# Performance work log

Hardware: AMD Instinct MI355X
Metric: run time of the kernel (lower is better)

Reference implementation:

```python
import jax, jax.numpy as jnp
import numpy as np

N = 65536          # query points (rays * samples per chunk)
C = 2048           # num_codes in code cloud
K = 16             # knn neighbors
CD = 64            # code_dim
IN_XYZ = 63        # positional-encoded xyz channels
IN_DIR = 27        # positional-encoded dir channels
W = 128            # decoder width (D=4, skips=[2])
DIST_SCALE = 2.0


def setup_inputs() -> dict:
    key = jax.random.key(0)
    ks = jax.random.split(key, 16)

    def glorot(k, shape):
        return jax.random.normal(k, shape, jnp.float32) / np.float32(np.sqrt(shape[0]))

    in_x = CD + IN_XYZ  # decoder in_channels_xyz = 127
    inp = {
        "indices": jnp.zeros((1,), jnp.int32),
        "query_points": jax.random.uniform(ks[0], (N, 3), jnp.float32),
        "xyzdir_embedded": jax.random.normal(ks[1], (N, IN_XYZ + IN_DIR), jnp.float32),
        "codes_position": jax.random.uniform(ks[2], (1, C, 3), jnp.float32),
        "codes": jax.random.normal(ks[3], (1, C, CD), jnp.float32) * 0.01,
        # decoder params
        "W0": glorot(ks[4], (in_x, W)), "b0": jnp.zeros((W,), jnp.float32),
        "W1": glorot(ks[5], (W, W)), "b1": jnp.zeros((W,), jnp.float32),
        "W2": glorot(ks[6], (W + in_x, W)), "b2": jnp.zeros((W,), jnp.float32),  # skip layer i=2
        "W3": glorot(ks[7], (W, W)), "b3": jnp.zeros((W,), jnp.float32),
        "Wf": glorot(ks[8], (W, W)), "bf": jnp.zeros((W,), jnp.float32),          # xyz_encoding_final
        "Wd": glorot(ks[9], (W + IN_DIR, W // 2)), "bd": jnp.zeros((W // 2,), jnp.float32),
        "Ws": glorot(ks[10], (W, 1)), "bs": jnp.zeros((1,), jnp.float32),
        "Wr": glorot(ks[11], (W // 2, 3)), "br": jnp.zeros((3,), jnp.float32),
    }
    return inp


def _knn_idx(q, c, k):
    # brute-force L2 knn (faiss replacement); indices only, no grad (torch no_grad)
    q = jax.lax.stop_gradient(q)
    c = jax.lax.stop_gradient(c)
    d2 = (jnp.sum(q * q, -1, keepdims=True)
          - 2.0 * q @ c.T
          + jnp.sum(c * c, -1))  # (N, C)
    _, idx = jax.lax.top_k(-d2, k)  # (N, K) nearest
    return idx


def reference(indices, query_points, xyzdir_embedded, codes_position, codes,
              W0, b0, W1, b1, W2, b2, W3, b3, Wf, bf, Wd, bd, Ws, bs, Wr, br):
    # --- CodeCloud.query ---
    cp = codes_position[indices][0]      # (C, 3)
    cc = codes[indices][0]               # (C, CD)
    idx = _knn_idx(query_points, cp, K)  # (N, K)
    neigh_pos = cp[idx]                  # (N, K, 3)
    sq = jnp.sum((query_points[:, None, :] - neigh_pos) ** 2, -1) + 1e-16  # (N, K)
    w = 1.0 / jnp.sqrt(sq) ** DIST_SCALE
    w = w / jnp.sum(w, -1, keepdims=True)
    neigh_codes = cc[idx]                # (N, K, CD)
    query_codes = jnp.einsum("nk,nkd->nd", w, neigh_codes)  # (N, CD)

    # --- IM_Decoder (D=4, W=128, skips=[2]) ---
    x = jnp.concatenate([query_codes, xyzdir_embedded], -1)  # (N, 127+27)
    in_x = CD + IN_XYZ
    input_xyz, input_dir = x[:, :in_x], x[:, in_x:]
    h = jax.nn.relu(input_xyz @ W0 + b0)
    h = jax.nn.relu(h @ W1 + b1)
    h = jax.nn.relu(jnp.concatenate([input_xyz, h], -1) @ W2 + b2)  # skip at i=2
    h = jax.nn.relu(h @ W3 + b3)
    sigma = h @ Ws + bs                       # (N, 1)
    final = h @ Wf + bf                       # (N, W)
    d = jax.nn.relu(jnp.concatenate([final, input_dir], -1) @ Wd + bd)
    rgb = d @ Wr + br                         # (N, 3)
    return jnp.concatenate([rgb, sigma], -1)  # (N, 4)
```

## Files before the change

kernel.cpp:

```cpp
#include <hip/hip_runtime.h>

#define N_Q   65536
#define N_C   2048
#define KNN_K 16
#define CDIM  64
#define SLCAP 64
#define KINF  0x7FFFFFFF

typedef _Float16 half_t;
typedef float v4f __attribute__((ext_vector_type(4)));
typedef half_t v8h __attribute__((ext_vector_type(8)));

#define ASTRIDE 136
#define DSTRIDE 40

__global__ void wtrans_kernel(const float* W0, const float* W1, const float* W2,
                              const float* W3, const float* Wf, const float* Wd,
                              const int* indices, const float* cpos,
                              half_t* wt, float4* cpos4){
  int idx = blockIdx.x * 256 + threadIdx.x;
  if (idx >= 110592) return;
  if (idx >= 108544){
    int i = idx - 108544;
    const float* cp = cpos + (size_t)indices[0] * N_C * 3;
    float x = cp[i*3 + 0], y = cp[i*3 + 1], z = cp[i*3 + 2];
    cpos4[i] = make_float4(x, y, z, fmaf(x, x, fmaf(y, y, fmaf(z, z, 4.0f))));
    return;
  }
  int base, nt, mode;
  const float* src = W1;
  if (idx < 16384){ base = 0; nt = 8; mode = 1; }
  else if (idx < 32768){ base = 16384; nt = 8; mode = 0; src = W1; }
  else if (idx < 65536){ base = 32768; nt = 8; mode = 2; }
  else if (idx < 81920){ base = 65536; nt = 8; mode = 0; src = W3; }
  else if (idx < 98304){ base = 81920; nt = 8; mode = 0; src = Wf; }
  else { base = 98304; nt = 4; mode = 3; }
  int i = idx - base;
  int tile = i >> 9, e = i & 511;
  int lane = e >> 3, j = e & 7;
  int k0idx = tile / nt, tcol = tile - k0idx*nt;
  int n = tcol*16 + (lane & 15);
  int k = k0idx*32 + ((lane >> 4) << 3) + j;
  float val;
  if (mode == 0)      val = src[k*128 + n];
  else if (mode == 1) val = (k < 127) ? W0[k*128 + n] : 0.f;
  else if (mode == 2) val = (k == 127) ? 0.f
                           : ((k < 127) ? W2[k*128 + n] : W2[(k-1)*128 + n]);
  else                val = (k < 155) ? Wd[k*64 + n] : 0.f;
  wt[idx] = (half_t)val;
}

__global__ void prep_kernel(const float* xyzdir, half_t* Ain, half_t* Din){
  int idx = blockIdx.x * 256 + threadIdx.x;
  if (idx < N_Q*72){
    int q = idx / 72, c = idx - q*72 + 64;
    float v = (c < 127) ? xyzdir[(size_t)q*90 + (c - 64)] : 0.f;
    Ain[(size_t)q*ASTRIDE + c] = (half_t)v;
  } else {
    int i2 = idx - N_Q*72;
    if (i2 >= N_Q*40) return;
    int q = i2 / 40, c = i2 - q*40;
    float v = (c < 27) ? xyzdir[(size_t)q*90 + 63 + c] : 0.f;
    Din[(size_t)q*DSTRIDE + c] = (half_t)v;
  }
}

__global__ __launch_bounds__(512, 8) void knn_kernel(const int* indices,
    const float* qpts, const float4* cpos4, const float* codes, half_t* Ain){
  __shared__ float4 lp[N_C];
  __shared__ int    sl[8*SLCAP];
  int tid = threadIdx.x;
  int lane = tid & 63, wave = tid >> 6;
  const float* cc = codes + (size_t)indices[0] * N_C * CDIM;

  for (int c = tid; c < N_C; c += 512) lp[c] = cpos4[c];
  __syncthreads();

  int q = blockIdx.x * 8 + wave;
  float qx = qpts[q*3 + 0];
  float qy = qpts[q*3 + 1];
  float qz = qpts[q*3 + 2];
  float nqx = -2.0f*qx, nqy = -2.0f*qy, nqz = -2.0f*qz;

  int p[32];
#pragma unroll
  for (int j = 0; j < 32; j++){
    int c = j*64 + lane;
    float4 P = lp[c];
    float s = fmaf(P.x, nqx, fmaf(P.y, nqy, fmaf(P.z, nqz, P.w)));
    p[j] = (__float_as_int(s) & 0xFFFFF800) | c;
  }

  int lm = p[0];
#pragma unroll
  for (int j = 1; j < 32; j++) lm = min(lm, p[j]);

  int v = lm;
#pragma unroll
  for (int k = 2; k <= 64; k <<= 1){
#pragma unroll
    for (int j = k >> 1; j > 0; j >>= 1){
      int o = __shfl_xor(v, j, 64);
      bool dirDesc = (lane & k) != 0;
      bool lower   = (lane & j) == 0;
      int mn = min(v, o), mx = max(v, o);
      v = (lower != dirDesc) ? mn : mx;
    }
  }
  int tau = __shfl(v, 15, 64);

  int cnt = 0;
#pragma unroll
  for (int j = 0; j < 32; j++) cnt += (p[j] <= tau) ? 1 : 0;
  int incl = cnt;
#pragma unroll
  for (int d = 1; d < 64; d <<= 1){
    int t = __shfl_up(incl, d, 64);
    incl += (lane >= d) ? t : 0;
  }
  int n = __shfl(incl, 63, 64);
  int base = incl - cnt;

  int keep = 0;
  if (n >= KNN_K && n <= SLCAP){
    int* slw = &sl[wave * SLCAP];
    int off = base;
#pragma unroll
    for (int j = 0; j < 32; j++){
      if (p[j] <= tau){ slw[off] = p[j]; off++; }
    }
    __builtin_amdgcn_wave_barrier();

    int x = (lane < n) ? slw[lane] : KINF;
#pragma unroll
    for (int k = 2; k <= 64; k <<= 1){
#pragma unroll
      for (int j = k >> 1; j > 0; j >>= 1){
        int o = __shfl_xor(x, j, 64);
        bool dirDesc = (lane & k) != 0;
        bool lower   = (lane & j) == 0;
        int mn = min(x, o), mx = max(x, o);
        x = (lower != dirDesc) ? mn : mx;
      }
    }
    keep = x;
  } else {
#pragma unroll 1
    for (int rr = 0; rr < KNN_K; rr++){
      int lmf = p[0];
#pragma unroll
      for (int j = 1; j < 32; j++) lmf = min(lmf, p[j]);
      int gm = lmf;
#pragma unroll
      for (int off2 = 1; off2 < 64; off2 <<= 1)
        gm = min(gm, __shfl_xor(gm, off2, 64));
      if (lane == rr) keep = gm;
#pragma unroll
      for (int j = 0; j < 32; j++) p[j] = (p[j] == gm) ? KINF : p[j];
    }
  }

  int ci = keep & 0x7FF;
  float4 P = lp[ci];
  float dx = qx - P.x, dy = qy - P.y, dz = qz - P.z;
  float d2 = fmaf(dz, dz, fmaf(dy, dy, dx*dx));
  float w = 1.0f / (d2 + 1e-16f);
  float wm = (lane < KNN_K) ? w : 0.0f;
#pragma unroll
  for (int off2 = 1; off2 < 64; off2 <<= 1) wm += __shfl_xor(wm, off2, 64);
  float wn = w / wm;

  float acc = 0.f;
#pragma unroll
  for (int i = 0; i < KNN_K; i++){
    int   cb = __shfl(ci, i, 64);
    float wb = __shfl(wn, i, 64);
    acc = fmaf(wb, cc[cb*CDIM + lane], acc);
  }
  Ain[(size_t)q*ASTRIDE + lane] = (half_t)acc;
}

template<int NT>
__device__ inline void mfma_sw(const half_t* act, int astride, int rowbase,
                               const half_t* wlayer, int nt, int ktbase,
                               int tcolbase, int kchunk, v4f* acc, int lane){
  int m = lane & 15, quad = lane >> 4;
#pragma unroll
  for (int k0 = 0; k0 < kchunk; k0 += 32){
    v8h a = *(const v8h*)&act[(rowbase + m)*astride + k0 + quad*8];
    int krow = ktbase + (k0 >> 5);
#pragma unroll
    for (int t = 0; t < NT; t++){
      const half_t* bp = wlayer + ((size_t)((krow*nt + tcolbase + t) << 9) + (lane << 3));
      v8h b = *(const v8h*)bp;
      acc[t] = __builtin_amdgcn_mfma_f32_16x16x32_f16(a, b, acc[t], 0, 0, 0);
    }
  }
}

template<int NT>
__device__ inline void epilogue(v4f* acc, half_t* outb, int rowbase, int colbase,
                                const float* bias, bool relu, int lane){
  int n = lane & 15, quad = lane >> 4;
#pragma unroll
  for (int t = 0; t < NT; t++){
    int col = colbase + t*16 + n;
    float bv = bias[col];
#pragma unroll
    for (int r = 0; r < 4; r++){
      float v = acc[t][r] + bv;
      if (relu) v = fmaxf(v, 0.f);
      outb[(rowbase + quad*4 + r)*ASTRIDE + col] = (half_t)v;
    }
  }
}

__global__ __launch_bounds__(256) void mlp_mfma(
    const half_t* Ain, const half_t* Din, const half_t* wt,
    const float* b0, const float* b1, const float* b2, const float* b3,
    const float* bfb, const float* bdb,
    const float* Wsb, const float* bsb, const float* Wrb, const float* brb,
    float* out){
  __shared__ __align__(16) half_t Abuf[32*ASTRIDE];
  __shared__ __align__(16) half_t Pbuf[32*ASTRIDE];
  __shared__ __align__(16) half_t Qbuf[32*ASTRIDE];
  __shared__ __align__(16) half_t Dbuf[32*DSTRIDE];

  int tid = threadIdx.x, lane = tid & 63, wave = tid >> 6;
  int qbase = blockIdx.x * 32;

  for (int i = tid; i < 32*17; i += 256){
    int r = i / 17, c8 = i - r*17;
    *(uint4*)&Abuf[r*ASTRIDE + (c8 << 3)] =
        *(const uint4*)&Ain[(size_t)(qbase + r)*ASTRIDE + (c8 << 3)];
  }
  for (int i = tid; i < 32*5; i += 256){
    int r = i / 5, c8 = i - r*5;
    *(uint4*)&Dbuf[r*DSTRIDE + (c8 << 3)] =
        *(const uint4*)&Din[(size_t)(qbase + r)*DSTRIDE + (c8 << 3)];
  }
  __syncthreads();

  int rowbase = (wave >> 1) * 16;
  int colhalf = wave & 1;
  int colbase = colhalf * 64;
  int tcolbase = colhalf * 4;
  v4f acc[4];

  const half_t* wt0 = wt;
  const half_t* wt1 = wt + 16384;
  const half_t* wt2 = wt + 32768;
  const half_t* wt3 = wt + 65536;
  const half_t* wtf = wt + 81920;
  const half_t* wtd = wt + 98304;

#define ZACC4() { for (int t_ = 0; t_ < 4; t_++) for (int e_ = 0; e_ < 4; e_++) acc[t_][e_] = 0.f; }

  ZACC4();
  mfma_sw<4>(Abuf, ASTRIDE, rowbase, wt0, 8, 0, tcolbase, 128, acc, lane);
  epilogue<4>(acc, Pbuf, rowbase, colbase, b0, true, lane);
  __syncthreads();

  ZACC4();
  mfma_sw<4>(Pbuf, ASTRIDE, rowbase, wt1, 8, 0, tcolbase, 128, acc, lane);
  epilogue<4>(acc, Qbuf, rowbase, colbase, b1, true, lane);
  __syncthreads();

  ZACC4();
  mfma_sw<4>(Abuf, ASTRIDE, rowbase, wt2, 8, 0, tcolbase, 128, acc, lane);
  mfma_sw<4>(Qbuf, ASTRIDE, rowbase, wt2, 8, 4, tcolbase, 128, acc, lane);
  epilogue<4>(acc, Pbuf, rowbase, colbase, b2, true, lane);
  __syncthreads();

  ZACC4();
  mfma_sw<4>(Pbuf, ASTRIDE, rowbase, wt3, 8, 0, tcolbase, 128, acc, lane);
  epilogue<4>(acc, Abuf, rowbase, colbase, b3, true, lane);
  __syncthreads();

  ZACC4();
  mfma_sw<4>(Abuf, ASTRIDE, rowbase, wtf, 8, 0, tcolbase, 128, acc, lane);
  epilogue<4>(acc, Pbuf, rowbase, colbase, bfb, false, lane);
  __syncthreads();

  int tcolbase_d = colhalf * 2;
  int colbase_d  = colhalf * 32;
  ZACC4();
  mfma_sw<2>(Pbuf, ASTRIDE, rowbase, wtd, 4, 0, tcolbase_d, 128, acc, lane);
  mfma_sw<2>(Dbuf, DSTRIDE, rowbase, wtd, 4, 4, tcolbase_d,  32, acc, lane);
  epilogue<2>(acc, Qbuf, rowbase, colbase_d, bdb, true, lane);
  __syncthreads();

  {
    int q = tid >> 3, part = tid & 7;
    float s = 0.f;
#pragma unroll
    for (int k = 0; k < 16; k++){
      int kk = part*16 + k;
      s = fmaf((float)Abuf[q*ASTRIDE + kk], Wsb[kk], s);
    }
    s += __shfl_xor(s, 1, 64); s += __shfl_xor(s, 2, 64); s += __shfl_xor(s, 4, 64);

    float r3[3];
#pragma unroll
    for (int c2 = 0; c2 < 3; c2++){
      float rv = 0.f;
#pragma unroll
      for (int k = 0; k < 8; k++){
        int kk = part*8 + k;
        rv = fmaf((float)Qbuf[q*ASTRIDE + kk], Wrb[kk*3 + c2], rv);
      }
      rv += __shfl_xor(rv, 1, 64); rv += __shfl_xor(rv, 2, 64); rv += __shfl_xor(rv, 4, 64);
      r3[c2] = rv;
    }
    if (part == 0){
      size_t ob = ((size_t)(qbase + q)) * 4;
      out[ob + 0] = r3[0] + brb[0];
      out[ob + 1] = r3[1] + brb[1];
      out[ob + 2] = r3[2] + brb[2];
      out[ob + 3] = s + bsb[0];
    }
  }
}

extern "C" void kernel_launch(void* const* d_in, const int* in_sizes, int n_in,
                              void* d_out, int out_size, void* d_ws, size_t ws_size,
                              hipStream_t stream){
  (void)in_sizes; (void)n_in; (void)out_size; (void)ws_size;

  const int*   indices = (const int*)d_in[0];
  const float* qpts    = (const float*)d_in[1];
  const float* xyzdir  = (const float*)d_in[2];
  const float* cpos    = (const float*)d_in[3];
  const float* codes   = (const float*)d_in[4];
  const float* W0 = (const float*)d_in[5];
  const float* b0 = (const float*)d_in[6];
  const float* W1 = (const float*)d_in[7];
  const float* b1 = (const float*)d_in[8];
  const float* W2 = (const float*)d_in[9];
  const float* b2 = (const float*)d_in[10];
  const float* W3 = (const float*)d_in[11];
  const float* b3 = (const float*)d_in[12];
  const float* Wf = (const float*)d_in[13];
  const float* bf = (const float*)d_in[14];
  const float* Wd = (const float*)d_in[15];
  const float* bd = (const float*)d_in[16];
  const float* Ws = (const float*)d_in[17];
  const float* bs = (const float*)d_in[18];
  const float* Wr = (const float*)d_in[19];
  const float* br = (const float*)d_in[20];

  half_t* Ain   = (half_t*)d_ws;
  half_t* Din   = (half_t*)((char*)d_ws + 17825792);
  half_t* wt    = (half_t*)((char*)d_ws + 17825792 + 5242880);
  float4* cpos4 = (float4*)((char*)d_ws + 17825792 + 5242880 + 217088);

  wtrans_kernel<<<(110592 + 255)/256, 256, 0, stream>>>(W0, W1, W2, W3, Wf, Wd,
                                                        indices, cpos, wt, cpos4);
  prep_kernel<<<(N_Q*112 + 255)/256, 256, 0, stream>>>(xyzdir, Ain, Din);
  knn_kernel<<<N_Q/8, 512, 0, stream>>>(indices, qpts, cpos4, codes, Ain);
  mlp_mfma<<<N_Q/32, 256, 0, stream>>>(Ain, Din, wt,
                                       b0, b1, b2, b3, bf, bd, Ws, bs, Wr, br,
                                       (float*)d_out);
}
```

Baseline: 243.1 us.

## Fuse input prep into knn kernel and cheapen threshold selection with ballot compaction

```diff
diff --git a/kernel.cpp b/kernel.cpp
--- a/kernel.cpp
+++ b/kernel.cpp
@@ -4,7 +4,7 @@
 #define N_C   2048
 #define KNN_K 16
 #define CDIM  64
-#define SLCAP 64
+#define SLCAP 128
 #define KINF  0x7FFFFFFF
 
 typedef _Float16 half_t;
@@ -50,27 +50,14 @@
   wt[idx] = (half_t)val;
 }
 
-__global__ void prep_kernel(const float* xyzdir, half_t* Ain, half_t* Din){
-  int idx = blockIdx.x * 256 + threadIdx.x;
-  if (idx < N_Q*72){
-    int q = idx / 72, c = idx - q*72 + 64;
-    float v = (c < 127) ? xyzdir[(size_t)q*90 + (c - 64)] : 0.f;
-    Ain[(size_t)q*ASTRIDE + c] = (half_t)v;
-  } else {
-    int i2 = idx - N_Q*72;
-    if (i2 >= N_Q*40) return;
-    int q = i2 / 40, c = i2 - q*40;
-    float v = (c < 27) ? xyzdir[(size_t)q*90 + 63 + c] : 0.f;
-    Din[(size_t)q*DSTRIDE + c] = (half_t)v;
-  }
-}
-
 __global__ __launch_bounds__(512, 8) void knn_kernel(const int* indices,
-    const float* qpts, const float4* cpos4, const float* codes, half_t* Ain){
+    const float* qpts, const float4* cpos4, const float* codes,
+    const float* xyzdir, half_t* Ain, half_t* Din){
   __shared__ float4 lp[N_C];
   __shared__ int    sl[8*SLCAP];
   int tid = threadIdx.x;
   int lane = tid & 63, wave = tid >> 6;
+  int l = lane & 15;
   const float* cc = codes + (size_t)indices[0] * N_C * CDIM;
 
   for (int c = tid; c < N_C; c += 512) lp[c] = cpos4[c];
@@ -97,54 +84,65 @@
 
   int v = lm;
 #pragma unroll
-  for (int k = 2; k <= 64; k <<= 1){
+  for (int k = 2; k <= 16; k <<= 1){
 #pragma unroll
     for (int j = k >> 1; j > 0; j >>= 1){
       int o = __shfl_xor(v, j, 64);
-      bool dirDesc = (lane & k) != 0;
-      bool lower   = (lane & j) == 0;
+      bool dirDesc = (l & k) != 0;
+      bool lower   = (l & j) == 0;
       int mn = min(v, o), mx = max(v, o);
       v = (lower != dirDesc) ? mn : mx;
     }
   }
-  int tau = __shfl(v, 15, 64);
-
-  int cnt = 0;
-#pragma unroll
-  for (int j = 0; j < 32; j++) cnt += (p[j] <= tau) ? 1 : 0;
-  int incl = cnt;
-#pragma unroll
-  for (int d = 1; d < 64; d <<= 1){
-    int t = __shfl_up(incl, d, 64);
-    incl += (lane >= d) ? t : 0;
-  }
-  int n = __shfl(incl, 63, 64);
-  int base = incl - cnt;
-
-  int keep = 0;
-  if (n >= KNN_K && n <= SLCAP){
-    int* slw = &sl[wave * SLCAP];
-    int off = base;
-#pragma unroll
-    for (int j = 0; j < 32; j++){
-      if (p[j] <= tau){ slw[off] = p[j]; off++; }
-    }
-    __builtin_amdgcn_wave_barrier();
-
+  int t0 = __shfl(v, 3, 64),  t1 = __shfl(v, 19, 64);
+  int t2 = __shfl(v, 35, 64), t3 = __shfl(v, 51, 64);
+  int tau = max(max(t0, t1), max(t2, t3));
+
+  int* slw = &sl[wave * SLCAP];
+  int n = 0;
+#pragma unroll
+  for (int j = 0; j < 32; j++){
+    bool c = (p[j] <= tau);
+    unsigned long long m = __ballot(c);
+    if (m){
+      if (n <= 64){
+        if (c){
+          int mb = __builtin_amdgcn_mbcnt_hi((unsigned)(m >> 32),
+                   __builtin_amdgcn_mbcnt_lo((unsigned)m, 0));
+          slw[n + mb] = p[j];
+        }
+      }
+      n += (int)__popcll(m);
+    }
+  }
+  __builtin_amdgcn_wave_barrier();
+
+  int keep;
+  if (n >= KNN_K && n <= 64){
     int x = (lane < n) ? slw[lane] : KINF;
 #pragma unroll
-    for (int k = 2; k <= 64; k <<= 1){
+    for (int k = 2; k <= 16; k <<= 1){
 #pragma unroll
       for (int j = k >> 1; j > 0; j >>= 1){
         int o = __shfl_xor(x, j, 64);
-        bool dirDesc = (lane & k) != 0;
-        bool lower   = (lane & j) == 0;
+        bool dirDesc = (l & k) != 0;
+        bool lower   = (l & j) == 0;
         int mn = min(x, o), mx = max(x, o);
         x = (lower != dirDesc) ? mn : mx;
       }
     }
+    x = min(x, __shfl_xor(x, 31, 64));
+#pragma unroll
+    for (int j = 8; j > 0; j >>= 1){
+      int o = __shfl_xor(x, j, 64);
+      bool lower = (l & j) == 0;
+      int mn = min(x, o), mx = max(x, o);
+      x = lower ? mn : mx;
+    }
+    x = min(x, __shfl_xor(x, 63, 64));
     keep = x;
   } else {
+    keep = KINF;
 #pragma unroll 1
     for (int rr = 0; rr < KNN_K; rr++){
       int lmf = p[0];
@@ -177,7 +175,16 @@
     float wb = __shfl(wn, i, 64);
     acc = fmaf(wb, cc[cb*CDIM + lane], acc);
   }
-  Ain[(size_t)q*ASTRIDE + lane] = (half_t)acc;
+  size_t arow = (size_t)q * ASTRIDE;
+  Ain[arow + lane] = (half_t)acc;
+
+  float xv = (lane < 63) ? xyzdir[(size_t)q*90 + lane] : 0.f;
+  Ain[arow + 64 + lane] = (half_t)xv;
+  if (lane < 8) Ain[arow + 128 + lane] = (half_t)0.f;
+  if (lane < 40){
+    float dv = (lane < 27) ? xyzdir[(size_t)q*90 + 63 + lane] : 0.f;
+    Din[(size_t)q*DSTRIDE + lane] = (half_t)dv;
+  }
 }
 
 template<int NT>
@@ -356,8 +363,8 @@
 
   wtrans_kernel<<<(110592 + 255)/256, 256, 0, stream>>>(W0, W1, W2, W3, Wf, Wd,
                                                         indices, cpos, wt, cpos4);
-  prep_kernel<<<(N_Q*112 + 255)/256, 256, 0, stream>>>(xyzdir, Ain, Din);
-  knn_kernel<<<N_Q/8, 512, 0, stream>>>(indices, qpts, cpos4, codes, Ain);
+  knn_kernel<<<N_Q/8, 512, 0, stream>>>(indices, qpts, cpos4, codes, xyzdir,
+                                        Ain, Din);
   mlp_mfma<<<N_Q/32, 256, 0, stream>>>(Ain, Din, wt,
                                        b0, b1, b2, b3, bf, bd, Ws, bs, Wr, br,
                                        (float*)d_out);
```

Measured after the change: 232.0 us. -4.6%, faster.
